# Optimization experiments

Measured on AMD Instinct MI355X. Metric: run time of the kernel, lower is better.

## Reference

```python
import jax, jax.numpy as jnp
import numpy as np

NUM_CLASSES = 21
POS_T, NEG_T, ALPHA, GAMMA, EPS = 0.5, 0.4, 0.25, 2.0, 1e-6
NEG_FILL = -1e30  # sorts below any focal value (focal >= 0)


def _pairwise_iou(a, b):
    # a: [A,4], b: [T,4] -> [A,T]
    x1 = jnp.maximum(a[:, None, 0], b[None, :, 0])
    y1 = jnp.maximum(a[:, None, 1], b[None, :, 1])
    x2 = jnp.minimum(a[:, None, 2], b[None, :, 2])
    y2 = jnp.minimum(a[:, None, 3], b[None, :, 3])
    inter = jnp.clip(x2 - x1, 0) * jnp.clip(y2 - y1, 0)
    a1 = (a[:, 2] - a[:, 0]) * (a[:, 3] - a[:, 1])
    a2 = (b[:, 2] - b[:, 0]) * (b[:, 3] - b[:, 1])
    return inter / (a1[:, None] + a2[None, :] - inter + EPS)


def _giou_loss(b1, b2):
    # b1, b2: [N,4] -> [N]
    x1 = jnp.maximum(b1[:, 0], b2[:, 0]); y1 = jnp.maximum(b1[:, 1], b2[:, 1])
    x2 = jnp.minimum(b1[:, 2], b2[:, 2]); y2 = jnp.minimum(b1[:, 3], b2[:, 3])
    inter = jnp.clip(x2 - x1, 0) * jnp.clip(y2 - y1, 0)
    a1 = (b1[:, 2] - b1[:, 0]) * (b1[:, 3] - b1[:, 1])
    a2 = (b2[:, 2] - b2[:, 0]) * (b2[:, 3] - b2[:, 1])
    union = a1 + a2 - inter
    iou = inter / (union + EPS)
    ex1 = jnp.minimum(b1[:, 0], b2[:, 0]); ey1 = jnp.minimum(b1[:, 1], b2[:, 1])
    ex2 = jnp.maximum(b1[:, 2], b2[:, 2]); ey2 = jnp.maximum(b1[:, 3], b2[:, 3])
    enc = (ex2 - ex1) * (ey2 - ey1)
    giou = iou - (enc - union) / (enc + EPS)
    return 1.0 - giou


def _per_image(conf, bbox, tb, tl, anchors):
    # conf: [A,C], bbox: [A,4], tb: [T,4], tl: [T], anchors: [A,4]
    A, C = conf.shape
    ious = _pairwise_iou(anchors, tb)                 # [A,T]
    max_ious = ious.max(axis=1)
    best_t = jnp.argmax(ious, axis=1)                 # [A] best target per anchor
    pos = max_ious >= POS_T
    neg = max_ious < NEG_T
    best_a = jnp.argmax(ious, axis=0)                 # [T] force-match best anchor per GT
    pos = pos.at[best_a].set(True)
    neg = neg.at[best_a].set(False)

    conf_target = jax.nn.one_hot(tl[best_t], C, dtype=conf.dtype) * pos[:, None].astype(conf.dtype)
    probs = jax.nn.softmax(conf, axis=1)
    is_pos_cell = conf_target == 1.0
    pt = jnp.where(is_pos_cell, probs, 1.0 - probs)
    alpha_f = jnp.where(is_pos_cell, ALPHA, 1.0 - ALPHA)
    focal = -alpha_f * (1.0 - pt) ** GAMMA * jnp.log(jnp.clip(pt, EPS))  # [A,C]

    num_pos = pos.sum()
    n_neg = neg.sum()
    pos_sum = jnp.where(pos[:, None], focal, 0.0).sum()

    # hard-negative mining: descending sort of masked flattened focal, sum top-k
    neg_flat = jnp.where(neg[:, None], focal, NEG_FILL).reshape(-1)
    sorted_neg = jnp.sort(neg_flat)[::-1]
    idx = jnp.arange(neg_flat.shape[0])
    k = jnp.minimum(3 * num_pos, n_neg)
    topk_sum = jnp.where(idx < k, sorted_neg, 0.0).sum()
    denom = jnp.maximum(num_pos + k, 1).astype(conf.dtype)
    conf_pos = jnp.where(n_neg > 0, (pos_sum + topk_sum) / denom,
                         pos_sum / jnp.maximum(num_pos, 1).astype(conf.dtype))

    k2 = jnp.minimum(100, n_neg)
    top2_mean = jnp.where(idx < k2, sorted_neg, 0.0).sum() / jnp.maximum(k2, 1).astype(conf.dtype)
    conf_nopos = jnp.where(n_neg > 0, top2_mean, focal.mean())
    conf_loss = jnp.where(num_pos > 0, conf_pos, conf_nopos)

    matched = tb[best_t]                              # [A,4]
    giou_l = _giou_loss(bbox, matched)                # [A]
    d = bbox - matched
    ad = jnp.abs(d)
    l1 = jnp.where(ad < 1.0, 0.5 * d * d, ad - 0.5).mean(axis=1)
    per = giou_l + 0.5 * l1
    bbox_loss = jnp.where(num_pos > 0,
                          jnp.where(pos, per, 0.0).sum() / jnp.maximum(num_pos, 1).astype(conf.dtype),
                          0.0)
    return conf_loss, bbox_loss


def _loss(conf_pred, bbox_pred, anchors, target_boxes, target_labels):
    conf_l, bbox_l = jax.vmap(
        lambda c, b, tb, tl: _per_image(c, b, tb, tl, anchors)
    )(conf_pred, bbox_pred, target_boxes, target_labels)
    conf_loss = conf_l.mean()
    bbox_loss = bbox_l.mean()
    total = 1.0 * conf_loss + 1.0 * bbox_loss  # conf_weight = bbox_weight = 1.0
    return jnp.stack([total, conf_loss, bbox_loss])


def _rand_boxes(key, shape):
    k1, k2 = jax.random.split(key)
    xy1 = jax.random.uniform(k1, shape + (2,)) * 0.8
    wh = jax.random.uniform(k2, shape + (2,)) * 0.2 + 0.01
    return jnp.concatenate([xy1, xy1 + wh], axis=-1)


def setup_inputs() -> dict:
    key = jax.random.key(0)
    ks = jax.random.split(key, 5)
    B, A, T, C = 16, 65536, 32, NUM_CLASSES
    conf_pred = jax.random.normal(ks[0], (B, A, C), dtype=jnp.float32)
    bbox_pred = _rand_boxes(ks[1], (B, A))
    anchors = _rand_boxes(ks[2], (A,))
    target_boxes = _rand_boxes(ks[3], (B, T))
    target_labels = jax.random.randint(ks[4], (B, T), 1, C)
    return {"conf_pred": conf_pred, "bbox_pred": bbox_pred, "anchors": anchors,
            "target_boxes": target_boxes, "target_labels": target_labels}


def reference(conf_pred, bbox_pred, anchors, target_boxes, target_labels):
    return _loss(conf_pred, bbox_pred, anchors, target_boxes, target_labels)
```

## Files before the change

### kernel.cpp

```cpp
#include <hip/hip_runtime.h>


#define AN 65536
#define BN 16
#define TN 32
#define CN 21
#define NBA 2048
#define LCAPG (2 * 65536)
#define LCAP 10240
#define CHUNK 256
#define BUFC (CHUNK * CN)

struct BlockAcc { float pos_sum; float bbox_sum; unsigned np; unsigned nn; };
struct ImgParams { double pos; double bbox; unsigned np, nn, k, ve, act; };

typedef float f4a __attribute__((ext_vector_type(4), aligned(4)));

__device__ __forceinline__ float box_area(float4 B) {
    return __fmul_rn(__fsub_rn(B.z, B.x), __fsub_rn(B.w, B.y));
}
__device__ __forceinline__ float iou_rcp(float4 A, float aa, float4 T, float ta) {
    float x1 = fmaxf(A.x, T.x), y1 = fmaxf(A.y, T.y);
    float x2 = fminf(A.z, T.z), y2 = fminf(A.w, T.w);
    float inter = __fmul_rn(fmaxf(__fsub_rn(x2, x1), 0.f), fmaxf(__fsub_rn(y2, y1), 0.f));
    float den = __fadd_rn(__fsub_rn(__fadd_rn(aa, ta), inter), 1e-6f);
    return __fmul_rn(inter, __builtin_amdgcn_rcpf(den));
}
__device__ __forceinline__ float row_prep_vals(float* __restrict__ c) {
    float m1[10];
#pragma unroll
    for (int j = 0; j < 10; ++j) m1[j] = fmaxf(c[j], c[j + 10]);
    float m2[5];
#pragma unroll
    for (int j = 0; j < 5; ++j) m2[j] = fmaxf(m1[j], m1[j + 5]);
    float ma = fmaxf(m2[0], m2[1]), mb = fmaxf(m2[2], m2[3]);
    float m = fmaxf(fmaxf(ma, mb), fmaxf(m2[4], c[20]));
#pragma unroll
    for (int j = 0; j < CN; ++j) c[j] = __expf(__fsub_rn(c[j], m));
    float s1[10];
#pragma unroll
    for (int j = 0; j < 10; ++j) s1[j] = __fadd_rn(c[j], c[j + 10]);
    float s2[5];
#pragma unroll
    for (int j = 0; j < 5; ++j) s2[j] = __fadd_rn(s1[j], s1[j + 5]);
    float sa = __fadd_rn(s2[0], s2[1]), sb = __fadd_rn(s2[2], s2[3]);
    float s = __fadd_rn(__fadd_rn(sa, sb), __fadd_rn(s2[4], c[20]));
    return __builtin_amdgcn_rcpf(s);
}
__device__ __forceinline__ float row_prep(const float* __restrict__ row, float* __restrict__ c) {
    const f4a* r4 = (const f4a*)row;
#pragma unroll
    for (int q = 0; q < 5; ++q) {
        f4a v = r4[q];
        c[q * 4 + 0] = v[0]; c[q * 4 + 1] = v[1];
        c[q * 4 + 2] = v[2]; c[q * 4 + 3] = v[3];
    }
    c[20] = row[20];
    return row_prep_vals(c);
}
__device__ __forceinline__ float cell_focal(float cexp, float inv, bool cellpos) {
    float p = __fmul_rn(cexp, inv);
    float pt = cellpos ? p : __fsub_rn(1.0f, p);
    float af = cellpos ? 0.25f : 0.75f;
    float om = __fsub_rn(1.0f, pt);
    float lg = __logf(fmaxf(pt, 1e-6f));
    return __fmul_rn(__fmul_rn(__fmul_rn(-af, om), om), lg);
}
__device__ __forceinline__ unsigned focal_bits(float fo) {
    unsigned bits = __float_as_uint(fo);
    if (bits == 0x80000000u) bits = 0u;
    return bits;
}
__device__ __forceinline__ float bbox_per(float4 b1, float4 b2) {
    float x1 = fmaxf(b1.x, b2.x), y1 = fmaxf(b1.y, b2.y);
    float x2 = fminf(b1.z, b2.z), y2 = fminf(b1.w, b2.w);
    float inter = fmaxf(x2 - x1, 0.f) * fmaxf(y2 - y1, 0.f);
    float a1 = (b1.z - b1.x) * (b1.w - b1.y);
    float a2 = (b2.z - b2.x) * (b2.w - b2.y);
    float un = a1 + a2 - inter;
    float iou = inter / (un + 1e-6f);
    float ex1 = fminf(b1.x, b2.x), ey1 = fminf(b1.y, b2.y);
    float ex2 = fmaxf(b1.z, b2.z), ey2 = fmaxf(b1.w, b2.w);
    float enc = (ex2 - ex1) * (ey2 - ey1);
    float giou = iou - (enc - un) / (enc + 1e-6f);
    float gl = 1.0f - giou;
    float l1 = 0.f, d, ad;
    d = b1.x - b2.x; ad = fabsf(d); l1 += (ad < 1.f) ? (0.5f * d * d) : (ad - 0.5f);
    d = b1.y - b2.y; ad = fabsf(d); l1 += (ad < 1.f) ? (0.5f * d * d) : (ad - 0.5f);
    d = b1.z - b2.z; ad = fabsf(d); l1 += (ad < 1.f) ? (0.5f * d * d) : (ad - 0.5f);
    d = b1.w - b2.w; ad = fabsf(d); l1 += (ad < 1.f) ? (0.5f * d * d) : (ad - 0.5f);
    return gl + 0.5f * (l1 * 0.25f);
}
__device__ __forceinline__ unsigned mbcnt64(unsigned long long m) {
    return __builtin_amdgcn_mbcnt_hi((unsigned)(m >> 32),
           __builtin_amdgcn_mbcnt_lo((unsigned)m, 0u));
}

__global__ __launch_bounds__(256) void main_kernel(
    const float* __restrict__ conf, const float4* __restrict__ bboxp,
    const float4* __restrict__ anchors, const float4* __restrict__ tboxes,
    const int* __restrict__ tlabels,
    unsigned long long* __restrict__ gbest,
    unsigned* __restrict__ ahist, unsigned short* __restrict__ maxb,
    BlockAcc* __restrict__ blockAcc)
{
    __shared__ float4 tbS[TN];
    __shared__ int tlS[TN];
    __shared__ float taS[TN];
    __shared__ float iouS[16][260];
    __shared__ unsigned ahp[NBA / 2];
    __shared__ float pbV[TN][8];
    __shared__ int   pbA[TN][8];
    __shared__ float rF[2][4];
    __shared__ unsigned rI[2][4];
    int b = blockIdx.y, tid = threadIdx.x;
    int a = blockIdx.x * 256 + tid;
    for (int i = tid; i < NBA / 2; i += 256) ahp[i] = 0u;
    if (tid < TN) {
        float4 T = tboxes[b * TN + tid];
        tbS[tid] = T; tlS[tid] = tlabels[b * TN + tid]; taS[tid] = box_area(T);
    }
    float4 ab = anchors[a];
    float aa = box_area(ab);
    __syncthreads();

    float best = -1.0f; int bt = 0;
#pragma unroll
    for (int h = 0; h < 2; ++h) {
#pragma unroll
        for (int t2 = 0; t2 < 16; ++t2) {
            int t = h * 16 + t2;
            float iou = iou_rcp(ab, aa, tbS[t], taS[t]);
            iouS[t2][tid] = iou;
            if (iou > best) { best = iou; bt = t; }
        }
        __syncthreads();
        if (tid < 128) {
            int t2 = tid & 15, pp = tid >> 4;
            const float4* rp = (const float4*)(&iouS[t2][pp * 32]);
            float bv = -1.f; int ba = 0;
#pragma unroll
            for (int q = 0; q < 8; ++q) {
                float4 v4 = rp[q];
                int i0 = pp * 32 + q * 4;
                if (v4.x > bv) { bv = v4.x; ba = i0 + 0; }
                if (v4.y > bv) { bv = v4.y; ba = i0 + 1; }
                if (v4.z > bv) { bv = v4.z; ba = i0 + 2; }
                if (v4.w > bv) { bv = v4.w; ba = i0 + 3; }
            }
            pbV[h * 16 + t2][pp] = bv; pbA[h * 16 + t2][pp] = ba;
        }
        __syncthreads();
    }
    if (tid < TN) {
        float bv = -1.f; int ba = 0;
#pragma unroll
        for (int pp = 0; pp < 8; ++pp) {
            float v = pbV[tid][pp];
            if (v > bv) { bv = v; ba = pbA[tid][pp]; }
        }
        unsigned ga = blockIdx.x * 256 + (unsigned)ba;
        unsigned long long key =
            (((unsigned long long)__float_as_uint(bv)) << 32) | (unsigned long long)(unsigned)(~ga);
        atomicMax(&gbest[b * TN + tid], key);
    }

    size_t idx = (size_t)b * AN + a;
    bool posA = best >= 0.5f;
    bool negA = best < 0.4f;
    float fs = 0.f, bper = 0.f;
    unsigned short mbenc = 0;
    if (posA || negA) {
        float c[CN];
        float inv = row_prep(conf + idx * CN, c);
        if (posA) {
            int label = tlS[bt];
#pragma unroll
            for (int j = 0; j < CN; ++j) fs += cell_focal(c[j], inv, j == label);
            bper = bbox_per(bboxp[idx], tbS[bt]);
        } else {
            float fo = cell_focal(1.0f, inv, false);
            unsigned bin = focal_bits(fo) >> 20;
            mbenc = (unsigned short)(bin + 1u);
            atomicAdd(&ahp[bin >> 1], 1u << ((bin & 1) << 4));
        }
    }
    maxb[idx] = mbenc;

    float vpos = posA ? fs : 0.f, vb = bper;
    unsigned inp = posA ? 1u : 0u, inn = negA ? 1u : 0u;
#pragma unroll
    for (int off = 32; off; off >>= 1) {
        vpos += __shfl_down(vpos, off, 64);
        vb   += __shfl_down(vb,   off, 64);
        inp  += __shfl_down(inp,  off, 64);
        inn  += __shfl_down(inn,  off, 64);
    }
    int wv = tid >> 6, ln = tid & 63;
    if (ln == 0) { rF[0][wv] = vpos; rF[1][wv] = vb; rI[0][wv] = inp; rI[1][wv] = inn; }
    __syncthreads();
    if (tid == 0) {
        BlockAcc ba2;
        ba2.pos_sum = rF[0][0] + rF[0][1] + rF[0][2] + rF[0][3];
        ba2.bbox_sum = rF[1][0] + rF[1][1] + rF[1][2] + rF[1][3];
        ba2.np = rI[0][0] + rI[0][1] + rI[0][2] + rI[0][3];
        ba2.nn = rI[1][0] + rI[1][1] + rI[1][2] + rI[1][3];
        blockAcc[b * 256 + blockIdx.x] = ba2;
    }
    for (int i = tid; i < NBA / 2; i += 256) {
        unsigned v = ahp[i];
        if (v) {
            if (v & 0xFFFFu) atomicAdd(&ahist[b * NBA + 2 * i], v & 0xFFFFu);
            if (v >> 16)     atomicAdd(&ahist[b * NBA + 2 * i + 1], v >> 16);
        }
    }
}

__global__ __launch_bounds__(1024) void tailA_kernel(
    const float* __restrict__ conf, const float4* __restrict__ bboxp,
    const float4* __restrict__ anchors, const float4* __restrict__ tboxes,
    const int* __restrict__ tlabels,
    const unsigned long long* __restrict__ gbest,
    const BlockAcc* __restrict__ blockAcc,
    const unsigned* __restrict__ ahist, unsigned short* __restrict__ maxb,
    ImgParams* __restrict__ params)
{
    __shared__ unsigned hist[NBA];
    __shared__ unsigned scan_[1024];
    __shared__ unsigned gaS[TN];
    __shared__ float4 tbS[TN];
    __shared__ int tlS[TN];
    __shared__ float taS[TN];
    __shared__ float dps[TN], dbb[TN];
    __shared__ int dnp[TN], dnn[TN];
    __shared__ double sdbl[16];
    __shared__ unsigned suns[16];
    __shared__ double s_pos, s_bbox;
    __shared__ unsigned s_np, s_nn, s_k, s_act, s_ve;

    int b = blockIdx.x, tid = threadIdx.x;
    int wv = tid >> 6, ln = tid & 63;

    for (int i = tid; i < NBA; i += 1024) hist[i] = ahist[b * NBA + i];
    if (tid < TN) {
        gaS[tid] = ~(unsigned)(gbest[b * TN + tid] & 0xFFFFFFFFull);
        float4 T = tboxes[b * TN + tid];
        tbS[tid] = T; tlS[tid] = tlabels[b * TN + tid]; taS[tid] = box_area(T);
        dps[tid] = 0.f; dbb[tid] = 0.f; dnp[tid] = 0; dnn[tid] = 0;
    }
    __syncthreads();

    if (tid < TN) {
        bool doit = true;
        unsigned ga = gaS[tid];
        for (int u = 0; u < tid; ++u) if (gaS[u] == ga) doit = false;
        if (doit) {
            size_t idx = (size_t)b * AN + ga;
            float4 ab = anchors[ga];
            float aa = box_area(ab);
            float best = -1.f; int bt = 0;
#pragma unroll
            for (int t = 0; t < TN; ++t) {
                float iou = iou_rcp(ab, aa, tbS[t], taS[t]);
                if (iou > best) { best = iou; bt = t; }
            }
            if (best < 0.5f) {
                int label = tlS[bt];
                float c[CN];
                float inv = row_prep(conf + idx * CN, c);
                float fsv = 0.f;
#pragma unroll
                for (int j = 0; j < CN; ++j) fsv += cell_focal(c[j], inv, j == label);
                dps[tid] = fsv;
                dbb[tid] = bbox_per(bboxp[idx], tbS[bt]);
                dnp[tid] = 1;
                if (best < 0.4f) {
                    unsigned enc = maxb[idx];
                    atomicSub(&hist[enc - 1u], 1u);
                    maxb[idx] = 0;
                    dnn[tid] = -1;
                }
            }
        }
    }
    __syncthreads();

    if (tid < 256) {
        BlockAcc ba = blockAcc[b * 256 + tid];
        double ps = (double)ba.pos_sum, bs = (double)ba.bbox_sum;
        unsigned np = ba.np, nn = ba.nn;
#pragma unroll
        for (int off = 32; off; off >>= 1) {
            ps += __shfl_down(ps, off, 64);
            bs += __shfl_down(bs, off, 64);
            np += __shfl_down(np, off, 64);
            nn += __shfl_down(nn, off, 64);
        }
        if (ln == 0) { sdbl[wv] = ps; sdbl[8 + wv] = bs; suns[wv] = np; suns[8 + wv] = nn; }
    }
    __syncthreads();
    if (tid == 0) {
        double dp = 0, db = 0; int cp = 0, cn = 0;
        for (int i = 0; i < TN; ++i) { dp += dps[i]; db += dbb[i]; cp += dnp[i]; cn += dnn[i]; }
        s_pos = sdbl[0] + sdbl[1] + sdbl[2] + sdbl[3] + dp;
        s_bbox = sdbl[8] + sdbl[9] + sdbl[10] + sdbl[11] + db;
        unsigned NP = (unsigned)((int)(suns[0] + suns[1] + suns[2] + suns[3]) + cp);
        unsigned NN = (unsigned)((int)(suns[8] + suns[9] + suns[10] + suns[11]) + cn);
        s_np = NP; s_nn = NN;
        unsigned k = min(3u * NP, NN);
        s_k = k;
        s_act = (NN > 0 && k > 0) ? 1u : 0u;
        s_ve = 0u;
    }
    __syncthreads();

    if (s_act) {
        unsigned k = s_k;
        unsigned lc0 = hist[tid * 2], lc1 = hist[tid * 2 + 1];
        unsigned cc = lc0 + lc1;
        scan_[tid] = cc;
        __syncthreads();
        for (int off = 1; off < 1024; off <<= 1) {
            unsigned v = (tid + off < 1024) ? scan_[tid + off] : 0u;
            __syncthreads();
            scan_[tid] += v;
            __syncthreads();
        }
        {
            unsigned above = (tid < 1023) ? scan_[tid + 1] : 0u;
            if (above < k && above + cc >= k) {
                unsigned bin = (above + lc1 >= k) ? (unsigned)(tid * 2 + 1) : (unsigned)(tid * 2);
                s_ve = (bin << 21) | 1u;
            }
        }
        __syncthreads();
    }
    if (tid == 0) {
        ImgParams P;
        P.pos = s_pos; P.bbox = s_bbox;
        P.np = s_np; P.nn = s_nn; P.k = s_k; P.ve = s_ve; P.act = s_act;
        params[b] = P;
    }
}

__global__ __launch_bounds__(256) void tailB_kernel(
    const float* __restrict__ conf, const unsigned short* __restrict__ maxb,
    const ImgParams* __restrict__ params,
    float* __restrict__ list, unsigned* __restrict__ listCnt)
{
    __shared__ int candS[1024];
    __shared__ unsigned bufS[BUFC];
    __shared__ unsigned s_cnt, s_bcnt, s_gbase;
    int b = blockIdx.y, tid = threadIdx.x;
    unsigned act = params[b].act;
    if (!act) return;
    unsigned ve = params[b].ve;
    unsigned vbits = ve >> 1;
    unsigned short tb16 = (unsigned short)((ve >> 21) + 1u);
    int base = blockIdx.x * 1024;

    if (tid == 0) s_cnt = 0u;
    __syncthreads();

    const ushort4* mb4 = (const ushort4*)(maxb + (size_t)b * AN + base);
    ushort4 m4 = mb4[tid];
    unsigned c0 = (m4.x >= tb16), c1 = (m4.y >= tb16), c2 = (m4.z >= tb16), c3 = (m4.w >= tb16);
    unsigned cnt = c0 + c1 + c2 + c3;
    unsigned pos = 0;
    if (cnt) pos = atomicAdd(&s_cnt, cnt);
    int a0 = base + tid * 4;
    if (c0) candS[pos++] = a0 + 0;
    if (c1) candS[pos++] = a0 + 1;
    if (c2) candS[pos++] = a0 + 2;
    if (c3) candS[pos++] = a0 + 3;
    __syncthreads();
    unsigned n = s_cnt;

    for (unsigned cbase = 0; cbase < n; cbase += CHUNK) {
        if (tid == 0) s_bcnt = 0u;
        __syncthreads();
        unsigned i = cbase + tid;
        if (i < n) {
            int a = candS[i];
            size_t idx = (size_t)b * AN + a;
            float c[CN];
            float inv = row_prep(conf + idx * CN, c);
#pragma unroll
            for (int j = 0; j < CN; ++j) {
                float fo = cell_focal(c[j], inv, false);
                unsigned bits = focal_bits(fo);
                bool hit = bits >= vbits;
                unsigned long long msk = __ballot(hit);
                if (hit) {
                    unsigned pre = mbcnt64(msk);
                    unsigned bb = 0;
                    if (pre == 0) bb = atomicAdd(&s_bcnt, (unsigned)__popcll(msk));
                    bb = __shfl(bb, (int)(__ffsll((long long)msk) - 1), 64);
                    bufS[bb + pre] = bits;
                }
            }
        }
        __syncthreads();
        unsigned ccnt = s_bcnt;
        if (ccnt) {
            if (tid == 0) s_gbase = atomicAdd(&listCnt[b * 16], ccnt);
            __syncthreads();
            unsigned gb = s_gbase;
            for (unsigned j2 = tid; j2 < ccnt; j2 += 256) {
                unsigned p = gb + j2;
                if (p < (unsigned)LCAPG)
                    list[(size_t)b * LCAPG + p] = __uint_as_float(bufS[j2]);
            }
        }
        __syncthreads();
    }
}

__global__ __launch_bounds__(1024) void tailC_kernel(
    const float* __restrict__ list, const unsigned* __restrict__ listCnt,
    const ImgParams* __restrict__ params,
    double* __restrict__ imgRes, unsigned* __restrict__ ctr,
    float* __restrict__ out)
{
    __shared__ float lcache[LCAP];
    __shared__ unsigned hist[4096];
    __shared__ unsigned scan_[1024];
    __shared__ double sdbl[16];
    __shared__ double s_sumAbove;
    __shared__ unsigned s_b1, s_rem, s_b2, s_rem2, s_b3, s_rem3;

    int b = blockIdx.x, tid = threadIdx.x;
    int wv = tid >> 6, ln = tid & 63;
    ImgParams P = params[b];
    double topk = 0.0;

    if (P.act) {
        unsigned n = min(listCnt[b * 16], (unsigned)LCAPG);
        const float* gl = list + (size_t)b * LCAPG;
        bool inL = (n <= (unsigned)LCAP);
        if (inL) for (unsigned i = tid; i < n; i += 1024) lcache[i] = gl[i];
        if (tid == 0) { s_b1 = 0; s_rem = 0; s_b3 = 0; s_rem3 = 0; }
        for (int i = tid; i < 4096; i += 1024) hist[i] = 0u;
        __syncthreads();

        for (unsigned i = tid; i < n; i += 1024) {
            unsigned bits = __float_as_uint(inL ? lcache[i] : gl[i]);
            atomicAdd(&hist[bits >> 20], 1u);
        }
        __syncthreads();

        unsigned lc0 = hist[tid * 2], lc1 = hist[tid * 2 + 1];
        unsigned cc = lc0 + lc1;
        scan_[tid] = cc;
        __syncthreads();
        for (int off = 1; off < 1024; off <<= 1) {
            unsigned v = (tid + off < 1024) ? scan_[tid + off] : 0u;
            __syncthreads();
            scan_[tid] += v;
            __syncthreads();
        }
        {
            unsigned total = scan_[0];
            unsigned above = (tid < 1023) ? scan_[tid + 1] : 0u;
            unsigned r = min(P.k, total);
            if (r > 0 && above < r && above + cc >= r) {
                if (above + lc1 >= r) { s_b1 = (unsigned)(tid * 2 + 1); s_rem = r - above; }
                else { s_b1 = (unsigned)(tid * 2); s_rem = r - above - lc1; }
            }
        }
        __syncthreads();
        unsigned b1 = s_b1, rem = s_rem;

        for (int i = tid; i < 4096; i += 1024) hist[i] = 0u;
        __syncthreads();
        double sA = 0.0;
        for (unsigned i = tid; i < n; i += 1024) {
            float v = inL ? lcache[i] : gl[i];
            unsigned bits = __float_as_uint(v);
            unsigned hi = bits >> 20;
            if (hi > b1) sA += (double)v;
            else if (hi == b1) atomicAdd(&hist[(bits >> 8) & 0xFFFu], 1u);
        }
#pragma unroll
        for (int off = 32; off; off >>= 1) sA += __shfl_down(sA, off, 64);
        if (ln == 0) sdbl[wv] = sA;
        __syncthreads();
        if (tid == 0) {
            double tt = 0;
            for (int w = 0; w < 16; ++w) tt += sdbl[w];
            s_sumAbove = tt;
        }
        __syncthreads();
        double sumAbove = s_sumAbove;

        if (rem == 0) {
            topk = sumAbove;
        } else {
            unsigned l4[4], cc4 = 0;
#pragma unroll
            for (int q = 0; q < 4; ++q) { l4[q] = hist[tid * 4 + q]; cc4 += l4[q]; }
            scan_[tid] = cc4;
            __syncthreads();
            for (int off = 1; off < 1024; off <<= 1) {
                unsigned v = (tid + off < 1024) ? scan_[tid + off] : 0u;
                __syncthreads();
                scan_[tid] += v;
                __syncthreads();
            }
            {
                unsigned total = scan_[0];
                unsigned above = (tid < 1023) ? scan_[tid + 1] : 0u;
                unsigned r = min(rem, total);
                if (above < r && above + cc4 >= r) {
                    unsigned a2 = above;
                    for (int i = 3; i >= 0; --i) {
                        unsigned bc = l4[i];
                        if (a2 + bc >= r) { s_b2 = (unsigned)(tid * 4 + i); s_rem2 = r - a2; break; }
                        a2 += bc;
                    }
                }
            }
            __syncthreads();
            unsigned b2 = s_b2, rem2 = s_rem2;
            if (tid < 256) hist[tid] = 0u;
            __syncthreads();

            double sMid = 0.0;
            for (unsigned i = tid; i < n; i += 1024) {
                float v = inL ? lcache[i] : gl[i];
                unsigned bits = __float_as_uint(v);
                if ((bits >> 20) != b1) continue;
                unsigned sub = (bits >> 8) & 0xFFFu;
                if (sub > b2) sMid += (double)v;
                else if (sub == b2) atomicAdd(&hist[bits & 0xFFu], 1u);
            }
            __syncthreads();
            if (tid < 256) scan_[tid] = hist[tid];
            __syncthreads();
            for (int off = 1; off < 256; off <<= 1) {
                unsigned v = 0;
                if (tid < 256 && tid + off < 256) v = scan_[tid + off];
                __syncthreads();
                if (tid < 256) scan_[tid] += v;
                __syncthreads();
            }
            if (tid < 256) {
                unsigned above8 = (tid < 255) ? scan_[tid + 1] : 0u;
                unsigned c8 = hist[tid];
                if (above8 < rem2 && above8 + c8 >= rem2) { s_b3 = (unsigned)tid; s_rem3 = rem2 - above8; }
            }
            __syncthreads();
            unsigned b3 = s_b3, rem3 = s_rem3;

            double s3 = 0.0;
            for (unsigned i = tid; i < n; i += 1024) {
                float v = inL ? lcache[i] : gl[i];
                unsigned bits = __float_as_uint(v);
                if ((bits >> 20) == b1 && ((bits >> 8) & 0xFFFu) == b2 && (bits & 0xFFu) > b3)
                    s3 += (double)v;
            }
            double tot = sMid + s3;
#pragma unroll
            for (int off = 32; off; off >>= 1) tot += __shfl_down(tot, off, 64);
            if (ln == 0) sdbl[wv] = tot;
            __syncthreads();
            if (tid == 0) {
                double totAll = 0;
                for (int w = 0; w < 16; ++w) totAll += sdbl[w];
                unsigned vb3 = (b1 << 20) | (b2 << 8) | b3;
                topk = sumAbove + totAll + (double)rem3 * (double)__uint_as_float(vb3);
            }
        }
    }

    if (tid == 0) {
        double confl;
        if (P.act) confl = (P.pos + topk) / (double)max(P.np + P.k, 1u);
        else       confl = P.pos / (double)max(P.np, 1u);
        imgRes[b * 2 + 0] = confl;
        imgRes[b * 2 + 1] = P.bbox / (double)max(P.np, 1u);
        __threadfence();
        unsigned prev = atomicAdd(ctr, 1u);
        if (prev == BN - 1) {
            __threadfence();
            double cs = 0, bs = 0;
            for (int i = 0; i < BN; ++i) { cs += imgRes[i * 2]; bs += imgRes[i * 2 + 1]; }
            cs /= BN; bs /= BN;
            out[0] = (float)(cs + bs);
            out[1] = (float)cs;
            out[2] = (float)bs;
        }
    }
}

extern "C" void kernel_launch(void* const* d_in, const int* in_sizes, int n_in,
                              void* d_out, int out_size, void* d_ws, size_t ws_size,
                              hipStream_t stream)
{
    (void)in_sizes; (void)n_in; (void)out_size; (void)ws_size;
    const float*  conf    = (const float*)d_in[0];
    const float4* bboxp   = (const float4*)d_in[1];
    const float4* anchors = (const float4*)d_in[2];
    const float4* tboxes  = (const float4*)d_in[3];
    const int*    tlabels = (const int*)d_in[4];
    float* out = (float*)d_out;
    char* ws = (char*)d_ws;
    size_t off = 0;
    auto alloc = [&](size_t bytes) -> void* {
        void* p = (void*)(ws + off);
        off = (off + bytes + 255) & ~(size_t)255;
        return p;
    };
    unsigned short* maxb = (unsigned short*)alloc((size_t)BN * AN * 2);
    float*     list     = (float*)alloc((size_t)BN * LCAPG * 4);
    BlockAcc*  blockAcc = (BlockAcc*)alloc((size_t)BN * 256 * sizeof(BlockAcc));
    double*    imgRes   = (double*)alloc((size_t)BN * 2 * 8);
    ImgParams* params   = (ImgParams*)alloc((size_t)BN * sizeof(ImgParams));
    size_t zstart = off;
    unsigned long long* gbest = (unsigned long long*)alloc((size_t)BN * TN * 8);
    unsigned* ahist   = (unsigned*)alloc((size_t)BN * NBA * 4);
    unsigned* ctr     = (unsigned*)alloc(256);
    unsigned* listCnt = (unsigned*)alloc((size_t)BN * 16 * 4);
    size_t zbytes = off - zstart;
    hipMemsetAsync(ws + zstart, 0, zbytes, stream);

    dim3 gridA(AN / 256, BN);
    main_kernel<<<gridA, 256, 0, stream>>>(conf, bboxp, anchors, tboxes, tlabels,
                                           gbest, ahist, maxb, blockAcc);
    tailA_kernel<<<BN, 1024, 0, stream>>>(conf, bboxp, anchors, tboxes, tlabels,
                                          gbest, blockAcc, ahist, maxb, params);
    tailB_kernel<<<dim3(64, BN), 256, 0, stream>>>(conf, maxb, params, list, listCnt);
    tailC_kernel<<<BN, 1024, 0, stream>>>(list, listCnt, params, imgRes, ctr, out);
}
```

Baseline: 202.1 us.

## Fuse per-image threshold selection into candidate-gathering kernel, recomputing it per block

```diff
diff --git a/kernel.cpp b/kernel.cpp
--- a/kernel.cpp
+++ b/kernel.cpp
@@ -216,38 +216,44 @@
     }
 }
 
-__global__ __launch_bounds__(1024) void tailA_kernel(
+__global__ __launch_bounds__(256) void tailB_kernel(
     const float* __restrict__ conf, const float4* __restrict__ bboxp,
     const float4* __restrict__ anchors, const float4* __restrict__ tboxes,
     const int* __restrict__ tlabels,
     const unsigned long long* __restrict__ gbest,
     const BlockAcc* __restrict__ blockAcc,
-    const unsigned* __restrict__ ahist, unsigned short* __restrict__ maxb,
-    ImgParams* __restrict__ params)
+    const unsigned* __restrict__ ahist, const unsigned short* __restrict__ maxb,
+    ImgParams* __restrict__ params,
+    float* __restrict__ list, unsigned* __restrict__ listCnt)
 {
     __shared__ unsigned hist[NBA];
-    __shared__ unsigned scan_[1024];
-    __shared__ unsigned gaS[TN];
+    __shared__ unsigned scanL[256];
     __shared__ float4 tbS[TN];
     __shared__ int tlS[TN];
     __shared__ float taS[TN];
+    __shared__ unsigned gaS[TN];
     __shared__ float dps[TN], dbb[TN];
     __shared__ int dnp[TN], dnn[TN];
-    __shared__ double sdbl[16];
-    __shared__ unsigned suns[16];
+    __shared__ unsigned undoS[TN], undoIR[TN];
+    __shared__ double sdblP[4], sdblB[4];
+    __shared__ unsigned sunsP[4], sunsB[4];
     __shared__ double s_pos, s_bbox;
-    __shared__ unsigned s_np, s_nn, s_k, s_act, s_ve;
-
-    int b = blockIdx.x, tid = threadIdx.x;
+    __shared__ unsigned s_np, s_nn, s_k, s_act, s_ve, s_undoCnt, s_irCnt;
+    __shared__ int candS[1024];
+    __shared__ unsigned bufS[BUFC];
+    __shared__ unsigned s_cnt, s_bcnt, s_gbase;
+
+    int b = blockIdx.y, tid = threadIdx.x;
     int wv = tid >> 6, ln = tid & 63;
 
-    for (int i = tid; i < NBA; i += 1024) hist[i] = ahist[b * NBA + i];
+    for (int i = tid; i < NBA; i += 256) hist[i] = ahist[b * NBA + i];
     if (tid < TN) {
         gaS[tid] = ~(unsigned)(gbest[b * TN + tid] & 0xFFFFFFFFull);
         float4 T = tboxes[b * TN + tid];
         tbS[tid] = T; tlS[tid] = tlabels[b * TN + tid]; taS[tid] = box_area(T);
         dps[tid] = 0.f; dbb[tid] = 0.f; dnp[tid] = 0; dnn[tid] = 0;
     }
+    if (tid == 0) { s_undoCnt = 0u; s_irCnt = 0u; s_cnt = 0u; }
     __syncthreads();
 
     if (tid < TN) {
@@ -277,15 +283,16 @@
                 if (best < 0.4f) {
                     unsigned enc = maxb[idx];
                     atomicSub(&hist[enc - 1u], 1u);
-                    maxb[idx] = 0;
                     dnn[tid] = -1;
+                    unsigned p = atomicAdd(&s_undoCnt, 1u);
+                    undoS[p] = ga;
                 }
             }
         }
     }
     __syncthreads();
 
-    if (tid < 256) {
+    {
         BlockAcc ba = blockAcc[b * 256 + tid];
         double ps = (double)ba.pos_sum, bs = (double)ba.bbox_sum;
         unsigned np = ba.np, nn = ba.nn;
@@ -296,16 +303,16 @@
             np += __shfl_down(np, off, 64);
             nn += __shfl_down(nn, off, 64);
         }
-        if (ln == 0) { sdbl[wv] = ps; sdbl[8 + wv] = bs; suns[wv] = np; suns[8 + wv] = nn; }
+        if (ln == 0) { sdblP[wv] = ps; sdblB[wv] = bs; sunsP[wv] = np; sunsB[wv] = nn; }
     }
     __syncthreads();
     if (tid == 0) {
         double dp = 0, db = 0; int cp = 0, cn = 0;
         for (int i = 0; i < TN; ++i) { dp += dps[i]; db += dbb[i]; cp += dnp[i]; cn += dnn[i]; }
-        s_pos = sdbl[0] + sdbl[1] + sdbl[2] + sdbl[3] + dp;
-        s_bbox = sdbl[8] + sdbl[9] + sdbl[10] + sdbl[11] + db;
-        unsigned NP = (unsigned)((int)(suns[0] + suns[1] + suns[2] + suns[3]) + cp);
-        unsigned NN = (unsigned)((int)(suns[8] + suns[9] + suns[10] + suns[11]) + cn);
+        s_pos = sdblP[0] + sdblP[1] + sdblP[2] + sdblP[3] + dp;
+        s_bbox = sdblB[0] + sdblB[1] + sdblB[2] + sdblB[3] + db;
+        unsigned NP = (unsigned)((int)(sunsP[0] + sunsP[1] + sunsP[2] + sunsP[3]) + cp);
+        unsigned NN = (unsigned)((int)(sunsB[0] + sunsB[1] + sunsB[2] + sunsB[3]) + cn);
         s_np = NP; s_nn = NN;
         unsigned k = min(3u * NP, NN);
         s_k = k;
@@ -316,59 +323,68 @@
 
     if (s_act) {
         unsigned k = s_k;
-        unsigned lc0 = hist[tid * 2], lc1 = hist[tid * 2 + 1];
-        unsigned cc = lc0 + lc1;
-        scan_[tid] = cc;
-        __syncthreads();
-        for (int off = 1; off < 1024; off <<= 1) {
-            unsigned v = (tid + off < 1024) ? scan_[tid + off] : 0u;
-            __syncthreads();
-            scan_[tid] += v;
+        unsigned l8[8], cc = 0;
+#pragma unroll
+        for (int q = 0; q < 8; ++q) { l8[q] = hist[tid * 8 + q]; cc += l8[q]; }
+        scanL[tid] = cc;
+        __syncthreads();
+        for (int off = 1; off < 256; off <<= 1) {
+            unsigned v = (tid + off < 256) ? scanL[tid + off] : 0u;
+            __syncthreads();
+            scanL[tid] += v;
             __syncthreads();
         }
         {
-            unsigned above = (tid < 1023) ? scan_[tid + 1] : 0u;
+            unsigned above = (tid < 255) ? scanL[tid + 1] : 0u;
             if (above < k && above + cc >= k) {
-                unsigned bin = (above + lc1 >= k) ? (unsigned)(tid * 2 + 1) : (unsigned)(tid * 2);
-                s_ve = (bin << 21) | 1u;
-            }
-        }
-        __syncthreads();
-    }
-    if (tid == 0) {
+                unsigned a2 = above;
+                for (int q = 7; q >= 0; --q) {
+                    unsigned bc = l8[q];
+                    if (a2 + bc >= k) { s_ve = ((unsigned)(tid * 8 + q) << 21) | 1u; break; }
+                    a2 += bc;
+                }
+            }
+        }
+        __syncthreads();
+    }
+    if (blockIdx.x == 0 && tid == 0) {
         ImgParams P;
         P.pos = s_pos; P.bbox = s_bbox;
         P.np = s_np; P.nn = s_nn; P.k = s_k; P.ve = s_ve; P.act = s_act;
         params[b] = P;
     }
-}
-
-__global__ __launch_bounds__(256) void tailB_kernel(
-    const float* __restrict__ conf, const unsigned short* __restrict__ maxb,
-    const ImgParams* __restrict__ params,
-    float* __restrict__ list, unsigned* __restrict__ listCnt)
-{
-    __shared__ int candS[1024];
-    __shared__ unsigned bufS[BUFC];
-    __shared__ unsigned s_cnt, s_bcnt, s_gbase;
-    int b = blockIdx.y, tid = threadIdx.x;
-    unsigned act = params[b].act;
-    if (!act) return;
-    unsigned ve = params[b].ve;
+    if (!s_act) return;
+
+    unsigned ve = s_ve;
     unsigned vbits = ve >> 1;
     unsigned short tb16 = (unsigned short)((ve >> 21) + 1u);
     int base = blockIdx.x * 1024;
 
-    if (tid == 0) s_cnt = 0u;
-    __syncthreads();
+    unsigned uc = s_undoCnt;
+    if (tid < uc) {
+        unsigned e = undoS[tid];
+        if (e >= (unsigned)base && e < (unsigned)(base + 1024)) {
+            unsigned p = atomicAdd(&s_irCnt, 1u);
+            undoIR[p] = e;
+        }
+    }
+    __syncthreads();
+    unsigned ir = s_irCnt;
 
     const ushort4* mb4 = (const ushort4*)(maxb + (size_t)b * AN + base);
     ushort4 m4 = mb4[tid];
     unsigned c0 = (m4.x >= tb16), c1 = (m4.y >= tb16), c2 = (m4.z >= tb16), c3 = (m4.w >= tb16);
+    int a0 = base + tid * 4;
+    for (unsigned u = 0; u < ir; ++u) {
+        unsigned e = undoIR[u];
+        if (e == (unsigned)a0)          c0 = 0;
+        else if (e == (unsigned)a0 + 1) c1 = 0;
+        else if (e == (unsigned)a0 + 2) c2 = 0;
+        else if (e == (unsigned)a0 + 3) c3 = 0;
+    }
     unsigned cnt = c0 + c1 + c2 + c3;
     unsigned pos = 0;
     if (cnt) pos = atomicAdd(&s_cnt, cnt);
-    int a0 = base + tid * 4;
     if (c0) candS[pos++] = a0 + 0;
     if (c1) candS[pos++] = a0 + 1;
     if (c2) candS[pos++] = a0 + 2;
@@ -627,8 +643,8 @@
     dim3 gridA(AN / 256, BN);
     main_kernel<<<gridA, 256, 0, stream>>>(conf, bboxp, anchors, tboxes, tlabels,
                                            gbest, ahist, maxb, blockAcc);
-    tailA_kernel<<<BN, 1024, 0, stream>>>(conf, bboxp, anchors, tboxes, tlabels,
-                                          gbest, blockAcc, ahist, maxb, params);
-    tailB_kernel<<<dim3(64, BN), 256, 0, stream>>>(conf, maxb, params, list, listCnt);
+    tailB_kernel<<<dim3(64, BN), 256, 0, stream>>>(conf, bboxp, anchors, tboxes, tlabels,
+                                                   gbest, blockAcc, ahist, maxb,
+                                                   params, list, listCnt);
     tailC_kernel<<<BN, 1024, 0, stream>>>(list, listCnt, params, imgRes, ctr, out);
 }
```

New measurement: 201.8 us, median of 2. About the same (-0.2%).
